# Kernel optimization log

Hardware: AMD Instinct MI355X
Metric: run time of the kernel (lower is better)

Reference implementation:

```python
import jax, jax.numpy as jnp
import numpy as np

B, L, DIM, GIN = 8, 2048, 512, 256
NFFT, HOP = 1024, 256
WIN = NFFT
OUT_DIM = NFFT + 2
PAD = (WIN - HOP) // 2  # 'same' padding trim
KS = 5  # dconv kernel size


def setup_inputs() -> dict:
    key = jax.random.key(0)
    ks = jax.random.split(key, 14)
    sd = lambda k, shape, s: jax.random.normal(k, shape, dtype=jnp.float32) * s
    return dict(
        x=jax.random.normal(ks[0], (B, DIM, L), dtype=jnp.float32),
        g_out=jax.random.normal(ks[1], (B, GIN, 1), dtype=jnp.float32),
        dconv_w=sd(ks[2], (DIM, 1, KS), 0.1),
        dconv_b=jnp.zeros((DIM,), jnp.float32),
        p1_w=sd(ks[3], (3 * DIM, DIM), 0.02),
        p1_b=jnp.zeros((3 * DIM,), jnp.float32),
        p1_ain=sd(ks[4], (DIM * 12, GIN), 0.01),
        p1_aout=sd(ks[5], (3 * DIM * 12, GIN), 1e-3),
        p2_w=sd(ks[6], (DIM, 3 * DIM), 0.02),
        p2_b=jnp.zeros((DIM,), jnp.float32),
        p2_ain=sd(ks[7], (3 * DIM * 12, GIN), 0.01),
        p2_aout=sd(ks[8], (DIM * 12, GIN), 1e-3),
        out_w=sd(ks[9], (OUT_DIM, DIM), 0.02),
        out_b=jnp.zeros((OUT_DIM,), jnp.float32),
        out_ain=sd(ks[10], (DIM * 16, GIN), 0.01),
        out_aout=sd(ks[11], (OUT_DIM * 16, GIN), 1e-3),
    )


def _dconv(x, w, b):
    # DilatedCausalConv1d: flip time, right-pad (k-1)*dilation, depthwise conv, flip back
    xf = jnp.flip(x, 2)
    xf = jnp.pad(xf, ((0, 0), (0, 0), (0, (KS - 1))))
    y = jax.lax.conv_general_dilated(
        xf, w, window_strides=(1,), padding='VALID',
        dimension_numbers=('NCH', 'OIH', 'NCH'), feature_group_count=DIM)
    y = y + b[None, :, None]
    return jnp.flip(y, 2)


def _lora(x, w, b, ain, aout, g, r):
    # main_fc: 1x1 conv == matmul over channels
    in_ch = x.shape[1]
    out_ch = w.shape[0]
    x_ = jnp.einsum('oi,bil->bol', w, x) + b[None, :, None]
    gv = g[:, :, 0]  # (B, gin)
    a_in = jnp.einsum('og,bg->bo', ain, gv).reshape(-1, in_ch, r)    # (B, in, r)
    a_out = jnp.einsum('og,bg->bo', aout, gv).reshape(-1, r, out_ch)  # (B, r, out)
    tmp = jnp.einsum('bcl,bcr->brl', x, a_in)
    return x_ + jnp.einsum('brl,brc->bcl', tmp, a_out)


def _istft_same(S):
    # S: (B, NFFT//2+1, T) complex
    Bn, _, T = S.shape
    n = jnp.arange(WIN)
    window = 0.5 * (1.0 - jnp.cos(2.0 * jnp.pi * n / WIN))  # periodic hann
    ifft = jnp.fft.irfft(S, n=NFFT, axis=1) * window[None, :, None]
    out_size = (T - 1) * HOP + WIN
    idx = (jnp.arange(T)[:, None] * HOP + n[None, :]).reshape(-1)
    frames = ifft.transpose(0, 2, 1).reshape(Bn, -1)
    y = jnp.zeros((Bn, out_size), frames.dtype).at[:, idx].add(frames)
    env = jnp.zeros((out_size,), frames.dtype).at[idx].add(jnp.tile(window ** 2, T))
    return y[:, PAD:-PAD] / env[PAD:-PAD]


def reference(x, g_out, dconv_w, dconv_b,
              p1_w, p1_b, p1_ain, p1_aout,
              p2_w, p2_b, p2_ain, p2_aout,
              out_w, out_b, out_ain, out_aout):
    h = _dconv(x, dconv_w, dconv_b)
    h = jax.nn.gelu(_lora(h, p1_w, p1_b, p1_ain, p1_aout, g_out, 12), approximate=False)
    h = jax.nn.gelu(_lora(h, p2_w, p2_b, p2_ain, p2_aout, g_out, 12), approximate=False)
    h = _lora(h, out_w, out_b, out_ain, out_aout, g_out, 16)
    mag, p = jnp.split(h, 2, axis=1)  # (B, NFFT//2+1, T) each
    mag = jnp.minimum(jnp.exp(mag), 100.0)
    S = mag * (jnp.cos(p) + 1j * jnp.sin(p))
    audio = _istft_same(S)
    return audio[:, None, :]  # (B, 1, T*HOP)
```

## Files before the change

kernel.cpp:

```cpp
#include <hip/hip_runtime.h>

#define L_SZ 2048
#define DIM_SZ 512
#define SPADK 1088
#define ATK 544
#define ATM 640
#define ATMV 576
#define ATSZ (ATM * ATK)
#define ATROW (2 * ATK)
#define ATSZ_PK (ATM * ATROW)

typedef __attribute__((ext_vector_type(8))) short bfx8;
typedef __attribute__((ext_vector_type(4))) float f32x4;

__device__ __forceinline__ ushort f2bf(float v) {
  unsigned u = __float_as_uint(v);
  unsigned r = u + 0x7FFFu + ((u >> 16) & 1u);
  return (ushort)(r >> 16);
}
__device__ __forceinline__ float bfhi_f(float v) {
  unsigned u = __float_as_uint(v);
  unsigned r = (u + 0x7FFFu + ((u >> 16) & 1u)) & 0xFFFF0000u;
  return __uint_as_float(r);
}

__device__ __forceinline__ void gl_lds16(const void* g, void* l) {
  __builtin_amdgcn_global_load_lds(
      (const __attribute__((address_space(1))) unsigned int*)(uintptr_t)g,
      (__attribute__((address_space(3))) unsigned int*)(uintptr_t)l, 16, 0, 0);
}

__device__ __forceinline__ void pk_store(ushort* base, size_t row, int pitch2k, int k,
                                         float v) {
  size_t o = row * (size_t)pitch2k + (size_t)((k >> 3) * 16 + (k & 7));
  float hf = bfhi_f(v);
  base[o] = (ushort)(__float_as_uint(hf) >> 16);
  base[o + 8] = f2bf(v - hf);
}

__global__ __launch_bounds__(256) void lora_vec_k(const float* __restrict__ mat, int rows,
                                                  const float* __restrict__ g,
                                                  float* __restrict__ out,
                                                  int tK, int tR) {
  __shared__ float gs[2048];
  int tid = threadIdx.x;
#pragma unroll
  for (int i = 0; i < 8; i++) gs[i * 256 + tid] = g[i * 256 + tid];
  __syncthreads();
  int row = blockIdx.x * 4 + (tid >> 6);
  if (row >= rows) return;
  int lane = tid & 63;
  float4 mv = *(const float4*)(mat + (size_t)row * 256 + lane * 4);
  float p[8];
#pragma unroll
  for (int b = 0; b < 8; b++) {
    const float* gb = gs + b * 256 + lane * 4;
    p[b] = mv.x * gb[0] + mv.y * gb[1] + mv.z * gb[2] + mv.w * gb[3];
  }
#pragma unroll
  for (int b = 0; b < 8; b++) {
    float v = p[b];
#pragma unroll
    for (int off = 32; off > 0; off >>= 1) v += __shfl_down(v, off, 64);
    if (lane == 0) {
      size_t o;
      if (tR > 0) {
        int kk = row / tR, rr = row - kk * tR;
        o = ((size_t)b * tR + rr) * tK + kk;
      } else {
        o = (size_t)b * rows + row;
      }
      out[o] = v;
    }
  }
}

__global__ __launch_bounds__(256) void weff_k(const float* __restrict__ W,
                                              const float* __restrict__ aint,
                                              const float* __restrict__ aout,
                                              ushort* __restrict__ opk, int M, int Mpad,
                                              int K, int R) {
  const int b = blockIdx.z;
  const int kc8 = K >> 3;
  int flat = blockIdx.x * 256 + threadIdx.x;
  int m = flat / kc8, kc = flat - m * kc8;
  float acc[8] = {};
  if (m < M) {
    const float4* wv = (const float4*)(W + (size_t)m * K + kc * 8);
    float4 w0 = wv[0], w1 = wv[1];
    acc[0] = w0.x; acc[1] = w0.y; acc[2] = w0.z; acc[3] = w0.w;
    acc[4] = w1.x; acc[5] = w1.y; acc[6] = w1.z; acc[7] = w1.w;
    const float* ai = aint + (size_t)b * R * K + kc * 8;
    const float* ao = aout + (size_t)b * M * R + m;
    for (int r = 0; r < R; r++) {
      float aor = ao[(size_t)r * M];
      const float4* av = (const float4*)(ai + (size_t)r * K);
      float4 a0 = av[0], a1 = av[1];
      acc[0] += aor * a0.x; acc[1] += aor * a0.y;
      acc[2] += aor * a0.z; acc[3] += aor * a0.w;
      acc[4] += aor * a1.x; acc[5] += aor * a1.y;
      acc[6] += aor * a1.z; acc[7] += aor * a1.w;
    }
  }
  unsigned hw[4], lw[4];
#pragma unroll
  for (int i = 0; i < 4; i++) {
    float h0 = bfhi_f(acc[2 * i]), h1 = bfhi_f(acc[2 * i + 1]);
    unsigned u0 = __float_as_uint(h0) >> 16, u1 = __float_as_uint(h1) >> 16;
    hw[i] = u0 | (u1 << 16);
    unsigned l0 = f2bf(acc[2 * i] - h0), l1 = f2bf(acc[2 * i + 1] - h1);
    lw[i] = l0 | (l1 << 16);
  }
  ushort* o = opk + ((size_t)b * Mpad + m) * (size_t)(2 * K) + kc * 16;
  *(uint4*)(o) = make_uint4(hw[0], hw[1], hw[2], hw[3]);
  *(uint4*)(o + 8) = make_uint4(lw[0], lw[1], lw[2], lw[3]);
}

__global__ __launch_bounds__(256) void dconv_k(const float* __restrict__ x,
                                               const float* __restrict__ w,
                                               const float* __restrict__ bias,
                                               ushort* __restrict__ h0pk) {
  const int t0 = blockIdx.x * 64;
  const int c0 = blockIdx.y * 64;
  const int b = blockIdx.z;
  const int tid = threadIdx.x;
  __shared__ float xs[64 * 68];
  const float* xb = x + ((size_t)b * DIM_SZ + c0) * L_SZ;
#pragma unroll
  for (int i = 0; i < 17; i++) {
    int flat = i * 256 + tid;
    int c = flat / 68, tt = flat % 68;
    int t = t0 - 4 + tt;
    xs[c * 68 + tt] = (t >= 0) ? xb[(size_t)c * L_SZ + t] : 0.0f;
  }
  __syncthreads();
  int c = tid & 63;
  int tb = (tid >> 6) * 16;
  float wl[5];
#pragma unroll
  for (int k = 0; k < 5; k++) wl[k] = w[(c0 + c) * 5 + k];
  float bl = bias[c0 + c];
#pragma unroll
  for (int j = 0; j < 16; j++) {
    int t = tb + j;
    float acc = bl;
#pragma unroll
    for (int k = 0; k < 5; k++) acc += wl[k] * xs[c * 68 + t + 4 - k];
    pk_store(h0pk, (size_t)b * L_SZ + t0 + t, 2 * DIM_SZ, c0 + c, acc);
  }
}

__global__ __launch_bounds__(256) void atab2_k(ushort* __restrict__ tab,
                                               double* __restrict__ win) {
  int flat = blockIdx.x * 256 + threadIdx.x;
  int table = flat / ATSZ;
  int rem = flat - table * ATSZ;
  int n = rem / ATK, k = rem % ATK;
  const double W = 6.283185307179586476925287 / 1024.0;
  float val = 0.f;
  if (n <= 512 && k <= 512) {
    double wn = 0.5 * (1.0 - cos(W * (double)n));
    int mm = (k * n) & 1023;
    if (table == 0) {
      double wk = (k == 0 || k == 512) ? 1.0 : 2.0;
      val = (float)(wn * wk * cos(W * (double)mm));
    } else {
      val = (float)(wn * 2.0 * sin(W * (double)mm));
    }
  }
  pk_store(tab + (size_t)table * ATSZ_PK, (size_t)n, ATROW, k, val);
  if (flat < 1024) win[flat] = 0.5 * (1.0 - cos(W * (double)flat));
}

__global__ __launch_bounds__(256) void sprep2_k(const float* __restrict__ mp,
                                                ushort* __restrict__ Sre,
                                                ushort* __restrict__ Sim) {
  size_t flat = (size_t)blockIdx.x * 256 + threadIdx.x;
  size_t row = flat / ATK;
  int k = (int)(flat % ATK);
  float re = 0.f, im = 0.f;
  if (k < 513) {
    const float* r = mp + row * SPADK;
    float m = r[k], p = r[513 + k];
    float mag = fminf(expf(m), 100.0f);
    re = mag * cosf(p);
    im = mag * sinf(p);
  }
  pk_store(Sre, row, ATROW, k, re);
  pk_store(Sim, row, ATROW, k, im);
}

template <bool GELU, bool OUTBF>
__global__ __launch_bounds__(256) void gemm_pk(
    const ushort* __restrict__ Apk, size_t a_bs,
    const ushort* __restrict__ Bpk, size_t b_bs,
    const float* __restrict__ bias, int Mb,
    float* __restrict__ Cf, ushort* __restrict__ Cpk, size_t c_bs, int ldc,
    int Mst, int K) {
  const int b = blockIdx.z;
  const int m0 = blockIdx.x * 128;
  const int t0 = blockIdx.y * 128;
  const int tid = threadIdx.x;
  const int l = tid & 63;
  const int w = tid >> 6;
  const int wm = (w & 1) * 64;
  const int wt = (w >> 1) * 64;
  const int tr = l & 15;
  const int ks = l >> 4;
  __shared__ ushort As[128 * 64];
  __shared__ ushort Bs[128 * 64];
  const int pitch = 2 * K;
  const int sr = l >> 3;
  const int sc = l & 7;
  const int scs = sc ^ sr;
  const ushort* gA = Apk + (size_t)b * a_bs + (size_t)(m0 + w * 32 + sr) * pitch + scs * 8;
  const ushort* gB = Bpk + (size_t)b * b_bs + (size_t)(t0 + w * 32 + sr) * pitch + scs * 8;
  ushort* lA = As + w * 32 * 64;
  ushort* lB = Bs + w * 32 * 64;
  const int swz = tr & 7;
  const int a_hi = (wm + tr) * 64 + (((2 * ks) ^ swz) * 8);
  const int a_lo = (wm + tr) * 64 + (((2 * ks + 1) ^ swz) * 8);
  const int b_hi = (wt + tr) * 64 + (((2 * ks) ^ swz) * 8);
  const int b_lo = (wt + tr) * 64 + (((2 * ks + 1) ^ swz) * 8);
  f32x4 acc[4][4];
#pragma unroll
  for (int i = 0; i < 4; i++)
#pragma unroll
    for (int j = 0; j < 4; j++) acc[i][j] = (f32x4){0.f, 0.f, 0.f, 0.f};
  for (int kt = 0; kt < K; kt += 32) {
    if (kt) __syncthreads();
    const ushort* ga = gA + kt * 2;
    const ushort* gb = gB + kt * 2;
#pragma unroll
    for (int i = 0; i < 4; i++) {
      gl_lds16(ga + (size_t)(i * 8) * pitch, lA + i * 8 * 64);
      gl_lds16(gb + (size_t)(i * 8) * pitch, lB + i * 8 * 64);
    }
    __syncthreads();
    bfx8 ah[4], bh[4], tl[4];
#pragma unroll
    for (int f = 0; f < 4; f++) ah[f] = *(const bfx8*)(As + a_hi + f * 1024);
#pragma unroll
    for (int f = 0; f < 4; f++) bh[f] = *(const bfx8*)(Bs + b_hi + f * 1024);
#pragma unroll
    for (int fi = 0; fi < 4; fi++)
#pragma unroll
      for (int fj = 0; fj < 4; fj++)
        acc[fi][fj] = __builtin_amdgcn_mfma_f32_16x16x32_bf16(ah[fi], bh[fj], acc[fi][fj], 0, 0, 0);
#pragma unroll
    for (int f = 0; f < 4; f++) tl[f] = *(const bfx8*)(Bs + b_lo + f * 1024);
#pragma unroll
    for (int fi = 0; fi < 4; fi++)
#pragma unroll
      for (int fj = 0; fj < 4; fj++)
        acc[fi][fj] = __builtin_amdgcn_mfma_f32_16x16x32_bf16(ah[fi], tl[fj], acc[fi][fj], 0, 0, 0);
#pragma unroll
    for (int f = 0; f < 4; f++) tl[f] = *(const bfx8*)(As + a_lo + f * 1024);
#pragma unroll
    for (int fi = 0; fi < 4; fi++)
#pragma unroll
      for (int fj = 0; fj < 4; fj++)
        acc[fi][fj] = __builtin_amdgcn_mfma_f32_16x16x32_bf16(tl[fi], bh[fj], acc[fi][fj], 0, 0, 0);
  }
  const int orow = ks * 4;
#pragma unroll
  for (int fi = 0; fi < 4; fi++) {
    int m = m0 + wm + fi * 16 + orow;
    if (m >= Mst) continue;
#pragma unroll
    for (int fj = 0; fj < 4; fj++) {
      int t = t0 + wt + fj * 16 + tr;
      float o[4];
#pragma unroll
      for (int i = 0; i < 4; i++) {
        float xv = acc[fi][fj][i];
        if (bias != nullptr && (m + i) < Mb) xv += bias[m + i];
        if (GELU) xv = 0.5f * xv * (1.0f + erff(xv * 0.70710678118654752f));
        o[i] = xv;
      }
      if (OUTBF) {
        size_t base = (size_t)b * c_bs + (size_t)t * (2 * ldc) + ((m >> 3) * 16 + (m & 7));
        ushort hb[4], lb[4];
#pragma unroll
        for (int i = 0; i < 4; i++) {
          float hf = bfhi_f(o[i]);
          hb[i] = (ushort)(__float_as_uint(hf) >> 16);
          lb[i] = f2bf(o[i] - hf);
        }
        *(ushort4*)(Cpk + base) = make_ushort4(hb[0], hb[1], hb[2], hb[3]);
        *(ushort4*)(Cpk + base + 8) = make_ushort4(lb[0], lb[1], lb[2], lb[3]);
      } else {
        *(float4*)(Cf + (size_t)b * c_bs + (size_t)t * ldc + m) =
            make_float4(o[0], o[1], o[2], o[3]);
      }
    }
  }
}

__global__ __launch_bounds__(256) void ola_k(const float* __restrict__ CD,
                                             const double* __restrict__ win,
                                             float* __restrict__ out) {
  size_t flat = (size_t)blockIdx.x * 256 + threadIdx.x;
  int b = (int)(flat >> 19);
  int t = (int)(flat & 524287);
  int g = t + 384;
  int r = g & 255, q4 = g >> 8;
  double acc = 0.0, env = 0.0;
#pragma unroll
  for (int q = 0; q < 4; q++) {
    int tau = q4 - q;
    int n = r + 256 * q;
    if (tau >= 0 && tau < 2048) {
      double w = win[n];
      int np = (n <= 512) ? n : 1024 - n;
      double sgn = (n <= 512) ? -1.0 : 1.0;
      const float* base = CD + ((size_t)b * 2048 + tau) * 1152 + np;
      acc += (double)base[0] + sgn * (double)base[576];
      env = fma(w, w, env);
    }
  }
  out[flat] = (float)(acc / (env * 1024.0));
}

extern "C" void kernel_launch(void* const* d_in, const int* in_sizes, int n_in, void* d_out,
                              int out_size, void* d_ws, size_t ws_size, hipStream_t stream) {
  (void)in_sizes; (void)n_in; (void)out_size; (void)ws_size;
  const float* x       = (const float*)d_in[0];
  const float* g_out   = (const float*)d_in[1];
  const float* dconv_w = (const float*)d_in[2];
  const float* dconv_b = (const float*)d_in[3];
  const float* p1_w    = (const float*)d_in[4];
  const float* p1_b    = (const float*)d_in[5];
  const float* p1_ain  = (const float*)d_in[6];
  const float* p1_aout = (const float*)d_in[7];
  const float* p2_w    = (const float*)d_in[8];
  const float* p2_b    = (const float*)d_in[9];
  const float* p2_ain  = (const float*)d_in[10];
  const float* p2_aout = (const float*)d_in[11];
  const float* out_w   = (const float*)d_in[12];
  const float* out_b   = (const float*)d_in[13];
  const float* out_ain = (const float*)d_in[14];
  const float* out_aout= (const float*)d_in[15];

  char* ws = (char*)d_ws;
  float* ain1  = (float*)(ws + 0);
  float* aout1 = (float*)(ws + 196608);
  float* ain2  = (float*)(ws + 786432);
  float* aout2 = (float*)(ws + 1376256);
  float* ain3  = (float*)(ws + 1572864);
  float* aout3 = (float*)(ws + 1835008);
  ushort* tab  = (ushort*)(ws + 2360320);
  double* win  = (double*)(ws + 5145600);
  char*  arena = ws + 5153792;
  ushort* h1  = (ushort*)(arena + 0);
  float*  mp  = (float*)(arena + 0);
  float*  CD  = (float*)(arena + 0);
  ushort* h0  = (ushort*)(arena + 100663296);
  ushort* h2  = (ushort*)(arena + 100663296);
  ushort* w1  = (ushort*)(arena + 134217728);
  ushort* w2  = (ushort*)(arena + 134217728);
  ushort* w3  = (ushort*)(arena + 134217728);
  ushort* Sre = (ushort*)(arena + 100663296);
  ushort* Sim = (ushort*)(arena + 136314880);

  lora_vec_k<<<1536, 256, 0, stream>>>(p1_ain, 6144, g_out, ain1, 512, 12);
  lora_vec_k<<<4608, 256, 0, stream>>>(p1_aout, 18432, g_out, aout1, 0, 0);
  lora_vec_k<<<4608, 256, 0, stream>>>(p2_ain, 18432, g_out, ain2, 1536, 12);
  lora_vec_k<<<1536, 256, 0, stream>>>(p2_aout, 6144, g_out, aout2, 0, 0);
  lora_vec_k<<<2048, 256, 0, stream>>>(out_ain, 8192, g_out, ain3, 512, 16);
  lora_vec_k<<<4104, 256, 0, stream>>>(out_aout, 16416, g_out, aout3, 0, 0);
  atab2_k<<<2720, 256, 0, stream>>>(tab, win);
  dconv_k<<<dim3(32, 8, 8), 256, 0, stream>>>(x, dconv_w, dconv_b, h0);

  weff_k<<<dim3(384, 1, 8), 256, 0, stream>>>(p1_w, ain1, aout1, w1, 1536, 1536, 512, 12);
  gemm_pk<true, true><<<dim3(12, 16, 8), 256, 0, stream>>>(
      w1, (size_t)1536 * 1024, h0, (size_t)2048 * 1024, p1_b, 1536,
      nullptr, h1, (size_t)2048 * 3072, 1536, 1536, 512);

  weff_k<<<dim3(384, 1, 8), 256, 0, stream>>>(p2_w, ain2, aout2, w2, 512, 512, 1536, 12);
  gemm_pk<true, true><<<dim3(4, 16, 8), 256, 0, stream>>>(
      w2, (size_t)512 * 3072, h1, (size_t)2048 * 3072, p2_b, 512,
      nullptr, h2, (size_t)2048 * 1024, 512, 512, 1536);

  weff_k<<<dim3(288, 1, 8), 256, 0, stream>>>(out_w, ain3, aout3, w3, 1026, 1152, 512, 16);
  gemm_pk<false, false><<<dim3(9, 16, 8), 256, 0, stream>>>(
      w3, (size_t)1152 * 1024, h2, (size_t)2048 * 1024, out_b, 1026,
      mp, nullptr, (size_t)2048 * SPADK, SPADK, SPADK, 512);

  sprep2_k<<<34816, 256, 0, stream>>>(mp, Sre, Sim);
  gemm_pk<false, false><<<dim3(5, 16, 8), 256, 0, stream>>>(
      tab, (size_t)0, Sre, (size_t)2048 * ATROW, nullptr, 0,
      CD, nullptr, (size_t)2048 * 1152, 1152, ATMV, ATK);
  gemm_pk<false, false><<<dim3(5, 16, 8), 256, 0, stream>>>(
      tab + ATSZ_PK, (size_t)0, Sim, (size_t)2048 * ATROW, nullptr, 0,
      CD + 576, nullptr, (size_t)2048 * 1152, 1152, ATMV, ATK);
  ola_k<<<16384, 256, 0, stream>>>(CD, win, (float*)d_out);
}
```

Measured before the change: 733.0 us.

## Double-buffer LDS tiles in packed GEMM to overlap global loads with MFMA

Splits the shared-memory A/B tiles into two buffers so the next K-tile is fetched with global-to-LDS loads while MFMAs run on the current one. Manual vmcnt waits and raw barriers replace the per-iteration __syncthreads pair, and s_setprio raises wave priority around the MFMA block. It also sets launch_bounds to request two blocks per CU. LDS use doubles to 64KB per block, which may limit occupancy, and the hand-written wait counts assume a fixed number of outstanding loads per stage.

```diff
diff --git a/kernel.cpp b/kernel.cpp
--- a/kernel.cpp
+++ b/kernel.cpp
@@ -191,7 +191,7 @@
 }
 
 template <bool GELU, bool OUTBF>
-__global__ __launch_bounds__(256) void gemm_pk(
+__global__ __launch_bounds__(256, 2) void gemm_pk(
     const ushort* __restrict__ Apk, size_t a_bs,
     const ushort* __restrict__ Bpk, size_t b_bs,
     const float* __restrict__ bias, int Mb,
@@ -207,61 +207,83 @@
   const int wt = (w >> 1) * 64;
   const int tr = l & 15;
   const int ks = l >> 4;
-  __shared__ ushort As[128 * 64];
-  __shared__ ushort Bs[128 * 64];
+  __shared__ ushort As[2][128 * 64];
+  __shared__ ushort Bs[2][128 * 64];
   const int pitch = 2 * K;
   const int sr = l >> 3;
   const int sc = l & 7;
   const int scs = sc ^ sr;
   const ushort* gA = Apk + (size_t)b * a_bs + (size_t)(m0 + w * 32 + sr) * pitch + scs * 8;
   const ushort* gB = Bpk + (size_t)b * b_bs + (size_t)(t0 + w * 32 + sr) * pitch + scs * 8;
-  ushort* lA = As + w * 32 * 64;
-  ushort* lB = Bs + w * 32 * 64;
   const int swz = tr & 7;
-  const int a_hi = (wm + tr) * 64 + (((2 * ks) ^ swz) * 8);
-  const int a_lo = (wm + tr) * 64 + (((2 * ks + 1) ^ swz) * 8);
-  const int b_hi = (wt + tr) * 64 + (((2 * ks) ^ swz) * 8);
-  const int b_lo = (wt + tr) * 64 + (((2 * ks + 1) ^ swz) * 8);
+  const int ch_hi = ((2 * ks) ^ swz) * 8;
+  const int ch_lo = ((2 * ks + 1) ^ swz) * 8;
+  const int aBase = (wm + tr) * 64;
+  const int bBase = (wt + tr) * 64;
+
+  auto stage = [&](int buf, int kel) {
+    const ushort* ga = gA + kel * 2;
+    const ushort* gb = gB + kel * 2;
+    ushort* la = As[buf] + w * 32 * 64;
+    ushort* lb = Bs[buf] + w * 32 * 64;
+#pragma unroll
+    for (int i = 0; i < 4; i++) {
+      gl_lds16(ga + (size_t)(i * 8) * pitch, la + i * 8 * 64);
+      gl_lds16(gb + (size_t)(i * 8) * pitch, lb + i * 8 * 64);
+    }
+  };
+
   f32x4 acc[4][4];
 #pragma unroll
   for (int i = 0; i < 4; i++)
 #pragma unroll
     for (int j = 0; j < 4; j++) acc[i][j] = (f32x4){0.f, 0.f, 0.f, 0.f};
-  for (int kt = 0; kt < K; kt += 32) {
-    if (kt) __syncthreads();
-    const ushort* ga = gA + kt * 2;
-    const ushort* gb = gB + kt * 2;
-#pragma unroll
-    for (int i = 0; i < 4; i++) {
-      gl_lds16(ga + (size_t)(i * 8) * pitch, lA + i * 8 * 64);
-      gl_lds16(gb + (size_t)(i * 8) * pitch, lB + i * 8 * 64);
-    }
-    __syncthreads();
+
+  const int NK = K / 32;
+  stage(0, 0);
+  int cur = 0;
+  for (int ki = 0; ki < NK; ki++) {
+    if (ki + 1 < NK) {
+      stage(cur ^ 1, (ki + 1) * 32);
+      asm volatile("s_waitcnt vmcnt(8)" ::: "memory");
+    } else {
+      asm volatile("s_waitcnt vmcnt(0)" ::: "memory");
+    }
+    __builtin_amdgcn_s_barrier();
+    __builtin_amdgcn_sched_barrier(0);
+    const ushort* Ac = As[cur];
+    const ushort* Bc = Bs[cur];
     bfx8 ah[4], bh[4], tl[4];
 #pragma unroll
-    for (int f = 0; f < 4; f++) ah[f] = *(const bfx8*)(As + a_hi + f * 1024);
-#pragma unroll
-    for (int f = 0; f < 4; f++) bh[f] = *(const bfx8*)(Bs + b_hi + f * 1024);
+    for (int f = 0; f < 4; f++) ah[f] = *(const bfx8*)(Ac + aBase + f * 1024 + ch_hi);
+#pragma unroll
+    for (int f = 0; f < 4; f++) bh[f] = *(const bfx8*)(Bc + bBase + f * 1024 + ch_hi);
+    __builtin_amdgcn_s_setprio(1);
 #pragma unroll
     for (int fi = 0; fi < 4; fi++)
 #pragma unroll
       for (int fj = 0; fj < 4; fj++)
         acc[fi][fj] = __builtin_amdgcn_mfma_f32_16x16x32_bf16(ah[fi], bh[fj], acc[fi][fj], 0, 0, 0);
 #pragma unroll
-    for (int f = 0; f < 4; f++) tl[f] = *(const bfx8*)(Bs + b_lo + f * 1024);
+    for (int f = 0; f < 4; f++) tl[f] = *(const bfx8*)(Bc + bBase + f * 1024 + ch_lo);
 #pragma unroll
     for (int fi = 0; fi < 4; fi++)
 #pragma unroll
       for (int fj = 0; fj < 4; fj++)
         acc[fi][fj] = __builtin_amdgcn_mfma_f32_16x16x32_bf16(ah[fi], tl[fj], acc[fi][fj], 0, 0, 0);
 #pragma unroll
-    for (int f = 0; f < 4; f++) tl[f] = *(const bfx8*)(As + a_lo + f * 1024);
+    for (int f = 0; f < 4; f++) tl[f] = *(const bfx8*)(Ac + aBase + f * 1024 + ch_lo);
 #pragma unroll
     for (int fi = 0; fi < 4; fi++)
 #pragma unroll
       for (int fj = 0; fj < 4; fj++)
         acc[fi][fj] = __builtin_amdgcn_mfma_f32_16x16x32_bf16(tl[fi], bh[fj], acc[fi][fj], 0, 0, 0);
-  }
+    __builtin_amdgcn_s_setprio(0);
+    __builtin_amdgcn_sched_barrier(0);
+    __builtin_amdgcn_s_barrier();
+    cur ^= 1;
+  }
+
   const int orow = ks * 4;
 #pragma unroll
   for (int fi = 0; fi < 4; fi++) {
```

Result: no change. 719.1 us (-1.9%).
